# Optimization experiments

Hardware: AMD Instinct MI355X
Metric: run time of the kernel (lower is better)

Reference implementation:

```python
import jax, jax.numpy as jnp
import numpy as np

N_QUBITS = 10


def setup_inputs() -> dict:
    key = jax.random.key(0)
    kx, kw = jax.random.split(key)
    # x: batch of rotation angles, last dim = n_qubits
    x = jax.random.normal(kx, (16384, 256, N_QUBITS), dtype=jnp.float32)
    # trainable per-qubit RY angles (nn.Parameter in the torch module)
    weights = jax.random.normal(kw, (N_QUBITS,), dtype=jnp.float32)
    return {"x": x, "weights": weights}


def reference(x, weights):
    """Exact analytic evaluation of the quantum circuit.

    Circuit: RX(x_i) on wire i, RY(w_i) on wire i, CNOT chain (0,1),(1,2),...,
    then expval(PauliZ(i)) on each wire.

    Derivation: pulling Z_i back through the CNOT chain (CNOT(c,t)^† Z_t
    CNOT(c,t) = Z_c Z_t) gives <Z_i> = <Z_0 Z_1 ... Z_i>. The pre-CNOT state
    is a product state, and for a single qubit RY(w)RX(x)|0> has
    <Z> = cos(x) cos(w). Hence out[..., i] = prod_{j<=i} cos(x_j) cos(w_j),
    i.e. a cumulative product along the qubit axis. This is bit-exact with
    the full state-vector simulation (up to float rounding).
    """
    per_qubit = jnp.cos(x) * jnp.cos(weights)  # [..., n_qubits], weights broadcast
    return jnp.cumprod(per_qubit, axis=-1)      # [..., n_qubits]
```

## Files before the change

kernel.cpp:

```cpp
#include <hip/hip_runtime.h>


#define BLOCK 256
#define ROWS_PER_THREAD 2
#define ROWS_PER_BLOCK (BLOCK * ROWS_PER_THREAD)
#define NQ 10
#define WORDS_PER_BLOCK (ROWS_PER_BLOCK * NQ)
#define U4_PER_BLOCK (WORDS_PER_BLOCK / 4)
#define U4_PER_THREAD (U4_PER_BLOCK / BLOCK)

__global__ __launch_bounds__(BLOCK) void qcircuit_kernel(
    const float* __restrict__ x,
    const float* __restrict__ w,
    float* __restrict__ out,
    int n_rows)
{
    __shared__ float4 buf4[U4_PER_BLOCK];
    float* bufw = (float*)buf4;

    const int tid = threadIdx.x;
    const long long block_row0 = (long long)blockIdx.x * ROWS_PER_BLOCK;
    const long long total_u4   = ((long long)n_rows * NQ) / 4;
    const long long u4_base    = (long long)blockIdx.x * U4_PER_BLOCK;
    const float4* __restrict__ gin  = (const float4*)x;
    float4* __restrict__       gout = (float4*)out;

    #pragma unroll
    for (int k = 0; k < U4_PER_THREAD; ++k) {
        long long gi = u4_base + (long long)(k * BLOCK + tid);
        if (gi < total_u4) buf4[k * BLOCK + tid] = gin[gi];
    }

    float cw[NQ];
    #pragma unroll
    for (int j = 0; j < NQ; ++j) cw[j] = __cosf(w[j]);

    __syncthreads();

    #pragma unroll
    for (int m = 0; m < ROWS_PER_THREAD; ++m) {
        const int r = tid + m * BLOCK;
        if (block_row0 + r < n_rows) {
            float v[NQ];
            #pragma unroll
            for (int j = 0; j < NQ; ++j) v[j] = bufw[r * NQ + j];
            float p = 1.0f;
            #pragma unroll
            for (int j = 0; j < NQ; ++j) {
                p *= __cosf(v[j]) * cw[j];
                v[j] = p;
            }
            #pragma unroll
            for (int j = 0; j < NQ; ++j) bufw[r * NQ + j] = v[j];
        }
    }

    __syncthreads();

    #pragma unroll
    for (int k = 0; k < U4_PER_THREAD; ++k) {
        long long gi = u4_base + (long long)(k * BLOCK + tid);
        if (gi < total_u4) gout[gi] = buf4[k * BLOCK + tid];
    }
}

extern "C" void kernel_launch(void* const* d_in, const int* in_sizes, int n_in,
                              void* d_out, int out_size, void* d_ws, size_t ws_size,
                              hipStream_t stream) {
    const float* x = (const float*)d_in[0];
    const float* w = (const float*)d_in[1];
    float* out = (float*)d_out;

    const int n_elem = in_sizes[0];
    const int n_rows = n_elem / NQ;
    const int blocks = (n_rows + ROWS_PER_BLOCK - 1) / ROWS_PER_BLOCK;

    hipLaunchKernelGGL(qcircuit_kernel, dim3(blocks), dim3(BLOCK), 0, stream,
                       x, w, out, n_rows);
}
```

Measured before the change: 284.0 us.

## Drop LDS staging; each thread loads two rows directly with nontemporal vector loads

Removes the shared-memory staging buffer and the two barriers. Each thread now reads a pair of rows (20 floats, 80 bytes aligned) straight from global memory as five 16-byte vectors, computes both cumulative products in registers, and writes them back with nontemporal stores. This avoids the LDS round trip and the synchronisation, but each thread's loads are strided by 80 bytes, so global coalescing across a wavefront is worse than the earlier fully contiguous block copy.

```diff
diff --git a/kernel.cpp b/kernel.cpp
--- a/kernel.cpp
+++ b/kernel.cpp
@@ -2,65 +2,47 @@
 
 
 #define BLOCK 256
-#define ROWS_PER_THREAD 2
-#define ROWS_PER_BLOCK (BLOCK * ROWS_PER_THREAD)
 #define NQ 10
-#define WORDS_PER_BLOCK (ROWS_PER_BLOCK * NQ)
-#define U4_PER_BLOCK (WORDS_PER_BLOCK / 4)
-#define U4_PER_THREAD (U4_PER_BLOCK / BLOCK)
+
+typedef float f32x4 __attribute__((ext_vector_type(4)));
 
 __global__ __launch_bounds__(BLOCK) void qcircuit_kernel(
     const float* __restrict__ x,
     const float* __restrict__ w,
     float* __restrict__ out,
-    int n_rows)
+    long long n_rows)
 {
-    __shared__ float4 buf4[U4_PER_BLOCK];
-    float* bufw = (float*)buf4;
-
-    const int tid = threadIdx.x;
-    const long long block_row0 = (long long)blockIdx.x * ROWS_PER_BLOCK;
-    const long long total_u4   = ((long long)n_rows * NQ) / 4;
-    const long long u4_base    = (long long)blockIdx.x * U4_PER_BLOCK;
-    const float4* __restrict__ gin  = (const float4*)x;
-    float4* __restrict__       gout = (float4*)out;
-
-    #pragma unroll
-    for (int k = 0; k < U4_PER_THREAD; ++k) {
-        long long gi = u4_base + (long long)(k * BLOCK + tid);
-        if (gi < total_u4) buf4[k * BLOCK + tid] = gin[gi];
-    }
+    const long long n_pairs = n_rows >> 1;
+    const long long p = (long long)blockIdx.x * BLOCK + threadIdx.x;
 
     float cw[NQ];
     #pragma unroll
     for (int j = 0; j < NQ; ++j) cw[j] = __cosf(w[j]);
 
-    __syncthreads();
+    if (p < n_pairs) {
+        const f32x4* __restrict__ gin  = (const f32x4*)x   + p * 5;
+        f32x4* __restrict__       gout = (f32x4*)out       + p * 5;
 
-    #pragma unroll
-    for (int m = 0; m < ROWS_PER_THREAD; ++m) {
-        const int r = tid + m * BLOCK;
-        if (block_row0 + r < n_rows) {
-            float v[NQ];
-            #pragma unroll
-            for (int j = 0; j < NQ; ++j) v[j] = bufw[r * NQ + j];
-            float p = 1.0f;
-            #pragma unroll
-            for (int j = 0; j < NQ; ++j) {
-                p *= __cosf(v[j]) * cw[j];
-                v[j] = p;
-            }
-            #pragma unroll
-            for (int j = 0; j < NQ; ++j) bufw[r * NQ + j] = v[j];
-        }
-    }
+        float v[20];
+        f32x4* vr = (f32x4*)v;
+        #pragma unroll
+        for (int k = 0; k < 5; ++k) vr[k] = __builtin_nontemporal_load(gin + k);
 
-    __syncthreads();
+        float pr = 1.0f;
+        #pragma unroll
+        for (int j = 0; j < NQ; ++j) { pr *= __cosf(v[j]) * cw[j]; v[j] = pr; }
+        pr = 1.0f;
+        #pragma unroll
+        for (int j = 0; j < NQ; ++j) { pr *= __cosf(v[NQ + j]) * cw[j]; v[NQ + j] = pr; }
 
-    #pragma unroll
-    for (int k = 0; k < U4_PER_THREAD; ++k) {
-        long long gi = u4_base + (long long)(k * BLOCK + tid);
-        if (gi < total_u4) gout[gi] = buf4[k * BLOCK + tid];
+        #pragma unroll
+        for (int k = 0; k < 5; ++k) __builtin_nontemporal_store(vr[k], gout + k);
+    } else if ((n_rows & 1) && p == n_pairs) {
+        const float* gi = x   + 2 * n_pairs * NQ;
+        float*       go = out + 2 * n_pairs * NQ;
+        float pr = 1.0f;
+        #pragma unroll
+        for (int j = 0; j < NQ; ++j) { pr *= __cosf(gi[j]) * cw[j]; go[j] = pr; }
     }
 }
 
@@ -71,9 +53,10 @@
     const float* w = (const float*)d_in[1];
     float* out = (float*)d_out;
 
-    const int n_elem = in_sizes[0];
-    const int n_rows = n_elem / NQ;
-    const int blocks = (n_rows + ROWS_PER_BLOCK - 1) / ROWS_PER_BLOCK;
+    const long long n_elem = in_sizes[0];
+    const long long n_rows = n_elem / NQ;
+    const long long n_work = (n_rows >> 1) + (n_rows & 1);
+    const int blocks = (int)((n_work + BLOCK - 1) / BLOCK);
 
     hipLaunchKernelGGL(qcircuit_kernel, dim3(blocks), dim3(BLOCK), 0, stream,
                        x, w, out, n_rows);
```

Result: slower. 518.0 us (+82.4%).
